# Optimization experiments

Hardware: AMD Instinct MI355X
Metric: run time of the kernel (lower is better)

The kernel has to match this reference:

```python
import jax, jax.numpy as jnp
import numpy as np

E = 1024      # embed_dim
QH = 16       # query heads
KVH = 4       # kv heads
HD = E // QH  # head_dim = 64
KVE = HD * KVH  # 256
EPS = 1e-5
ROPE_BASE = 10000.0


def rope(x, d):
    # Faithful to the source RoPE: d == number of heads (x.shape[-2]),
    # and the 'sequence' axis of the cache is x.shape[0] (the batch dim).
    # rope(x) = x*cos + (x*sin) * neg_half(x)  (note: nonlinear in x).
    b = x.shape[0]
    theta = 1.0 / (ROPE_BASE ** (jnp.arange(0, d, 2, dtype=jnp.float32) / d))  # (d//2,)
    seq_idx = jnp.arange(b, dtype=jnp.float32)                                 # (b,)
    idx_theta = seq_idx[:, None] * theta[None, :]                              # (b, d//2)
    idx2 = jnp.concatenate([idx_theta, idx_theta], axis=-1)                    # (b, d)
    # cached shape (b,1,1,d); source permutes (0,1,3,2) -> (b,1,d,1)
    cos = jnp.cos(idx2)[:, None, :, None]  # (b,1,d,1)
    sin = jnp.sin(idx2)[:, None, :, None]
    d2 = d // 2
    # split of the LAST dim (head_dim) at d//2 == num_heads//2, as in source
    neg = jnp.concatenate([-x[..., d2:], x[..., :d2]], axis=-1)
    return x * cos + (x * sin) * neg


def setup_inputs() -> dict:
    key = jax.random.key(0)
    ks = jax.random.split(key, 12)
    b, n = 1, 2048

    def xavier(k, shape):
        fan_out, fan_in = shape
        std = (2.0 / (fan_in + fan_out)) ** 0.5
        return jax.random.normal(k, shape, dtype=jnp.float32) * std

    return {
        "query": jax.random.normal(ks[0], (b, n, E), dtype=jnp.float32),
        "key": jax.random.normal(ks[1], (b, n, E), dtype=jnp.float32),
        "value": jax.random.normal(ks[2], (b, n, E), dtype=jnp.float32),
        "Wq": xavier(ks[3], (E, E)),
        "bq": jnp.zeros((E,), jnp.float32),
        "Wk": xavier(ks[4], (KVE, E)),
        "bk": jnp.zeros((KVE,), jnp.float32),
        "Wv": xavier(ks[5], (KVE, E)),
        "bv": jnp.zeros((KVE,), jnp.float32),
        "gamma": jnp.ones((E,), jnp.float32),
        "beta": jnp.zeros((E,), jnp.float32),
    }


def reference(query, key, value, Wq, bq, Wk, bk, Wv, bv, gamma, beta):
    b, n, _ = query.shape
    q = query @ Wq.T + bq            # (b,n,E)
    k = key @ Wk.T + bk              # (b,n,KVE)
    v = value @ Wv.T + bv            # (b,n,KVE)

    q = q.reshape(b, n, QH, HD)      # b n h d
    k = k.reshape(b, n, KVH, HD)
    v = v.reshape(b, n, KVH, HD)

    q = rope(q, QH)
    k = rope(k, KVH)

    # b n h d -> b h n d
    q = jnp.transpose(q, (0, 2, 1, 3))
    k = jnp.transpose(k, (0, 2, 1, 3))
    v = jnp.transpose(v, (0, 2, 1, 3))

    scale = float(HD) ** 0.5
    q = q / scale

    g = QH // KVH
    # 'b (h g) n d -> b g h n d' : h outer, g inner
    q = q.reshape(b, KVH, g, n, HD)              # (b, h, g, n, d)
    q = jnp.transpose(q, (0, 2, 1, 3, 4))        # (b, g, h, n, d)

    sim = jnp.einsum('bghnd,bhsd->bghns', q, k)  # (b,g,h,n,s)
    attn = jax.nn.softmax(sim, axis=-1)
    out = jnp.einsum('bghns,bhsd->bghnd', attn, v)

    # 'b g h n d -> b n (h g) d'
    out = jnp.transpose(out, (0, 3, 2, 1, 4))    # (b, n, h, g, d)
    x = out.reshape(b, n, QH * HD)               # (b, n, E)

    # LayerNorm (biased variance, as in torch)
    mu = jnp.mean(x, axis=-1, keepdims=True)
    var = jnp.mean((x - mu) ** 2, axis=-1, keepdims=True)
    x = (x - mu) * jax.lax.rsqrt(var + EPS) * gamma + beta

    # NOTE: source computes out_proj(x) but returns x, so out_proj is dead code.
    return x
```

## Files before the change

kernel.cpp:

```cpp
#include <hip/hip_runtime.h>
#include <math.h>

#define EDIM   1024
#define KVEDIM 256
#define HDIM   64
#define QHEADS 16

typedef __attribute__((ext_vector_type(8))) short short8;
typedef __attribute__((ext_vector_type(4))) float f32x4;

__device__ __forceinline__ unsigned pack2(float a, float b) {
    unsigned ua = __builtin_bit_cast(unsigned, a);
    unsigned ub = __builtin_bit_cast(unsigned, b);
    ua += 0x7fffu + ((ua >> 16) & 1u);
    ub += 0x7fffu + ((ub >> 16) & 1u);
    return (ua >> 16) | (ub & 0xffff0000u);
}
__device__ __forceinline__ short f2b(float a) {
    unsigned ua = __builtin_bit_cast(unsigned, a);
    ua += 0x7fffu + ((ua >> 16) & 1u);
    return (short)(ua >> 16);
}

__global__ __launch_bounds__(256)
void cvt_bf16(const float* __restrict__ s0, const float* __restrict__ s1,
              const float* __restrict__ s2, const float* __restrict__ s3,
              const float* __restrict__ s4, const float* __restrict__ s5,
              short* __restrict__ d0, short* __restrict__ d1,
              short* __restrict__ d2, short* __restrict__ d3,
              short* __restrict__ d4, short* __restrict__ d5,
              int n0, int n1, int n2, int n3, int n4, int n5)
{
    const float* s; short* d; int n;
    switch (blockIdx.y) {
        case 0: s = s0; d = d0; n = n0; break;
        case 1: s = s1; d = d1; n = n1; break;
        case 2: s = s2; d = d2; n = n2; break;
        case 3: s = s3; d = d3; n = n3; break;
        case 4: s = s4; d = d4; n = n4; break;
        default: s = s5; d = d5; n = n5; break;
    }
    int i = ((int)blockIdx.x * 256 + threadIdx.x) * 8;
    if (i >= n) return;
    float4 a = *(const float4*)&s[i];
    float4 b = *(const float4*)&s[i + 4];
    uint4 o;
    o.x = pack2(a.x, a.y); o.y = pack2(a.z, a.w);
    o.z = pack2(b.x, b.y); o.w = pack2(b.z, b.w);
    *(uint4*)&d[i] = o;
}

__global__ __launch_bounds__(256)
void proj_gemm(const short* __restrict__ Aq, const short* __restrict__ Ak,
               const short* __restrict__ Av,
               const short* __restrict__ Wqb, const short* __restrict__ Wkb,
               const short* __restrict__ Wvb,
               const float* __restrict__ bq, const float* __restrict__ bk,
               const float* __restrict__ bv,
               short* __restrict__ Cq, short* __restrict__ Ck,
               short* __restrict__ Cv, float qscale)
{
    const int bid = blockIdx.x;
    const short* A; const short* W; const float* bias; short* C;
    int N, bm, bn; float scale;
    if (bid < 128) {
        A = Aq; W = Wqb; bias = bq; C = Cq; N = EDIM; scale = qscale;
        bm = (bid >> 3) * 128; bn = (bid & 7) * 128;
    } else if (bid < 160) {
        int i = bid - 128;
        A = Ak; W = Wkb; bias = bk; C = Ck; N = KVEDIM; scale = 1.0f;
        bm = (i >> 1) * 128; bn = (i & 1) * 128;
    } else {
        int i = bid - 160;
        A = Av; W = Wvb; bias = bv; C = Cv; N = KVEDIM; scale = 1.0f;
        bm = (i >> 1) * 128; bn = (i & 1) * 128;
    }
    const int K = EDIM;

    __shared__ short As[128 * 72];
    __shared__ short Ws[128 * 72];

    const int t = threadIdx.x, lane = t & 63, wv = t >> 6;
    const int lm = lane & 15, quad = lane >> 4;
    const int q8 = quad * 8, q4 = quad * 4;
    const int wm = (wv & 1) * 64, wn = (wv >> 1) * 64;
    const int sr = t >> 3, sc = (t & 7) * 8;

    f32x4 zero = {0.f, 0.f, 0.f, 0.f};
    f32x4 acc[4][4];
    #pragma unroll
    for (int i = 0; i < 4; ++i)
        #pragma unroll
        for (int j = 0; j < 4; ++j) acc[i][j] = zero;

    for (int k0 = 0; k0 < K; k0 += 64) {
        __syncthreads();
        #pragma unroll
        for (int i = 0; i < 4; ++i) {
            int r = sr + i * 32;
            *(uint4*)&As[r * 72 + sc] = *(const uint4*)&A[(size_t)(bm + r) * K + k0 + sc];
            *(uint4*)&Ws[r * 72 + sc] = *(const uint4*)&W[(size_t)(bn + r) * K + k0 + sc];
        }
        __syncthreads();
        #pragma unroll
        for (int ks = 0; ks < 2; ++ks) {
            short8 af[4], bfr[4];
            #pragma unroll
            for (int i = 0; i < 4; ++i)
                af[i] = *(const short8*)&As[(wm + i * 16 + lm) * 72 + ks * 32 + q8];
            #pragma unroll
            for (int j = 0; j < 4; ++j)
                bfr[j] = *(const short8*)&Ws[(wn + j * 16 + lm) * 72 + ks * 32 + q8];
            #pragma unroll
            for (int i = 0; i < 4; ++i)
                #pragma unroll
                for (int j = 0; j < 4; ++j)
                    acc[i][j] = __builtin_amdgcn_mfma_f32_16x16x32_bf16(
                        af[i], bfr[j], acc[i][j], 0, 0, 0);
        }
    }

    #pragma unroll
    for (int j = 0; j < 4; ++j) {
        float bj = bias[bn + wn + j * 16 + lm];
        #pragma unroll
        for (int i = 0; i < 4; ++i)
            #pragma unroll
            for (int r = 0; r < 4; ++r)
                C[(size_t)(bm + wm + i * 16 + q4 + r) * N + bn + wn + j * 16 + lm] =
                    f2b((acc[i][j][r] + bj) * scale);
    }
}

__global__ __launch_bounds__(256)
void attn_mfma(const short* __restrict__ q, const short* __restrict__ k,
               const short* __restrict__ v, float* __restrict__ x, int n)
{
    __shared__ short Ks[64 * 72];
    __shared__ short Vt[64 * 72];
    __shared__ short Ps[64 * 72];
    __shared__ float Lred[4][64];

    const int qh = blockIdx.y, kvh = qh >> 2;
    const int r0 = blockIdx.x * 64;
    const int t = threadIdx.x;
    const int lane = t & 63, wv = t >> 6;
    const int lm = lane & 15, quad = lane >> 4;
    const int q8 = quad * 8, q4 = quad * 4;

    short8 qf[4][2];
    #pragma unroll
    for (int qt = 0; qt < 4; ++qt) {
        const short* qrow = &q[(size_t)(r0 + qt * 16 + lm) * EDIM + qh * HDIM];
        qf[qt][0] = *(const short8*)&qrow[q8];
        qf[qt][1] = *(const short8*)&qrow[32 + q8];
    }

    const int rt0 = (wv & 1) * 2;
    const int dt0 = (wv >> 1) * 2;

    f32x4 zero = {0.f, 0.f, 0.f, 0.f};
    f32x4 oacc[2][2];
    #pragma unroll
    for (int i = 0; i < 2; ++i)
        #pragma unroll
        for (int j = 0; j < 2; ++j) oacc[i][j] = zero;
    float lp[4] = {0.f, 0.f, 0.f, 0.f};

    const int krow = t >> 2, kc = (t & 3) * 8;
    const int vs4 = (t & 15) * 4, vd0 = (t >> 4) * 4;

    for (int s0 = 0; s0 < n; s0 += 64) {
        __syncthreads();
        {
            const uint4* ksrc = (const uint4*)&k[(size_t)(s0 + krow) * KVEDIM + kvh * HDIM];
            uint4 ka = ksrc[t & 3];
            uint4 kb = ksrc[(t & 3) + 4];
            *(uint4*)&Ks[krow * 72 + kc] = ka;
            *(uint4*)&Ks[krow * 72 + kc + 32] = kb;
        }
        {
            unsigned vr[4][2];
            #pragma unroll
            for (int i = 0; i < 4; ++i) {
                uint2 vv = *(const uint2*)&v[(size_t)(s0 + vs4 + i) * KVEDIM + kvh * HDIM + vd0];
                vr[i][0] = vv.x; vr[i][1] = vv.y;
            }
            #pragma unroll
            for (int j = 0; j < 4; ++j) {
                int w = j >> 1, hi = (j & 1) * 16;
                unsigned e0 = (vr[0][w] >> hi) & 0xffffu;
                unsigned e1 = (vr[1][w] >> hi) & 0xffffu;
                unsigned e2 = (vr[2][w] >> hi) & 0xffffu;
                unsigned e3 = (vr[3][w] >> hi) & 0xffffu;
                uint2 o; o.x = e0 | (e1 << 16); o.y = e2 | (e3 << 16);
                *(uint2*)&Vt[(vd0 + j) * 72 + vs4] = o;
            }
        }
        __syncthreads();

        short8 kf0 = *(const short8*)&Ks[(wv * 16 + lm) * 72 + q8];
        short8 kf1 = *(const short8*)&Ks[(wv * 16 + lm) * 72 + 32 + q8];
        #pragma unroll
        for (int qt = 0; qt < 4; ++qt) {
            f32x4 s = zero;
            s = __builtin_amdgcn_mfma_f32_16x16x32_bf16(kf0, qf[qt][0], s, 0, 0, 0);
            s = __builtin_amdgcn_mfma_f32_16x16x32_bf16(kf1, qf[qt][1], s, 0, 0, 0);
            float p0 = exp2f(s[0]);
            float p1 = exp2f(s[1]);
            float p2 = exp2f(s[2]);
            float p3 = exp2f(s[3]);
            lp[qt] += (p0 + p1) + (p2 + p3);
            uint2 pw; pw.x = pack2(p0, p1); pw.y = pack2(p2, p3);
            *(uint2*)&Ps[(qt * 16 + lm) * 72 + wv * 16 + q4] = pw;
        }
        __syncthreads();

        short8 vf[2][2];
        #pragma unroll
        for (int j = 0; j < 2; ++j) {
            vf[j][0] = *(const short8*)&Vt[((dt0 + j) * 16 + lm) * 72 + q8];
            vf[j][1] = *(const short8*)&Vt[((dt0 + j) * 16 + lm) * 72 + 32 + q8];
        }
        #pragma unroll
        for (int i = 0; i < 2; ++i) {
            short8 pf0 = *(const short8*)&Ps[((rt0 + i) * 16 + lm) * 72 + q8];
            short8 pf1 = *(const short8*)&Ps[((rt0 + i) * 16 + lm) * 72 + 32 + q8];
            #pragma unroll
            for (int j = 0; j < 2; ++j) {
                oacc[i][j] = __builtin_amdgcn_mfma_f32_16x16x32_bf16(pf0, vf[j][0], oacc[i][j], 0, 0, 0);
                oacc[i][j] = __builtin_amdgcn_mfma_f32_16x16x32_bf16(pf1, vf[j][1], oacc[i][j], 0, 0, 0);
            }
        }
    }

    #pragma unroll
    for (int qt = 0; qt < 4; ++qt) {
        float l = lp[qt];
        l += __shfl_xor(l, 16);
        l += __shfl_xor(l, 32);
        if (lane < 16) Lred[wv][qt * 16 + lm] = l;
    }
    __syncthreads();

    #pragma unroll
    for (int i = 0; i < 2; ++i) {
        #pragma unroll
        for (int r = 0; r < 4; ++r) {
            int row = (rt0 + i) * 16 + q4 + r;
            float lsum = (Lred[0][row] + Lred[1][row]) + (Lred[2][row] + Lred[3][row]);
            float inv = 1.0f / lsum;
            #pragma unroll
            for (int j = 0; j < 2; ++j)
                x[(size_t)(r0 + row) * EDIM + qh * HDIM + (dt0 + j) * 16 + lm] =
                    oacc[i][j][r] * inv;
        }
    }
}

__global__ __launch_bounds__(256)
void ln_kernel(float* __restrict__ x, const float* __restrict__ gamma,
               const float* __restrict__ beta)
{
    const int rowbase = (int)blockIdx.x * EDIM;
    const int t = threadIdx.x;

    float4 xv = *(const float4*)&x[rowbase + t * 4];
    float s  = xv.x + xv.y + xv.z + xv.w;
    float sq = xv.x * xv.x + xv.y * xv.y + xv.z * xv.z + xv.w * xv.w;
    #pragma unroll
    for (int m = 1; m < 64; m <<= 1) {
        s  += __shfl_xor(s,  m);
        sq += __shfl_xor(sq, m);
    }
    __shared__ float ws_[4], wq_[4];
    const int wave = t >> 6;
    if ((t & 63) == 0) { ws_[wave] = s; wq_[wave] = sq; }
    __syncthreads();
    s  = ws_[0] + ws_[1] + ws_[2] + ws_[3];
    sq = wq_[0] + wq_[1] + wq_[2] + wq_[3];

    const float mu   = s * (1.f / EDIM);
    const float var  = sq * (1.f / EDIM) - mu * mu;
    const float rstd = rsqrtf(var + 1e-5f);

    float4 g = *(const float4*)&gamma[t * 4];
    float4 b = *(const float4*)&beta[t * 4];
    float4 o;
    o.x = (xv.x - mu) * rstd * g.x + b.x;
    o.y = (xv.y - mu) * rstd * g.y + b.y;
    o.z = (xv.z - mu) * rstd * g.z + b.z;
    o.w = (xv.w - mu) * rstd * g.w + b.w;
    *(float4*)&x[rowbase + t * 4] = o;
}

extern "C" void kernel_launch(void* const* d_in, const int* in_sizes, int n_in,
                              void* d_out, int out_size, void* d_ws, size_t ws_size,
                              hipStream_t stream)
{
    const float* query = (const float*)d_in[0];
    const float* key   = (const float*)d_in[1];
    const float* value = (const float*)d_in[2];
    const float* Wq    = (const float*)d_in[3];
    const float* bq    = (const float*)d_in[4];
    const float* Wk    = (const float*)d_in[5];
    const float* bk    = (const float*)d_in[6];
    const float* Wv    = (const float*)d_in[7];
    const float* bv    = (const float*)d_in[8];
    const float* gamma = (const float*)d_in[9];
    const float* beta  = (const float*)d_in[10];
    float* out = (float*)d_out;

    const int n = in_sizes[0] / EDIM;

    short* qa  = (short*)d_ws;
    short* ka  = qa  + (size_t)n * EDIM;
    short* va  = ka  + (size_t)n * EDIM;
    short* wqb = va  + (size_t)n * EDIM;
    short* wkb = wqb + (size_t)EDIM * EDIM;
    short* wvb = wkb + (size_t)KVEDIM * EDIM;
    short* qb  = wvb + (size_t)KVEDIM * EDIM;
    short* kb  = qb  + (size_t)n * EDIM;
    short* vb  = kb  + (size_t)n * KVEDIM;

    const float qscale = 0.125f * 1.44269504088896f;

    cvt_bf16<<<dim3(1024, 6), 256, 0, stream>>>(
        query, key, value, Wq, Wk, Wv,
        qa, ka, va, wqb, wkb, wvb,
        n * EDIM, n * EDIM, n * EDIM, EDIM * EDIM, KVEDIM * EDIM, KVEDIM * EDIM);

    proj_gemm<<<dim3(192), 256, 0, stream>>>(
        qa, ka, va, wqb, wkb, wvb, bq, bk, bv, qb, kb, vb, qscale);

    attn_mfma<<<dim3(n / 64, QHEADS), 256, 0, stream>>>(qb, kb, vb, out, n);

    ln_kernel<<<dim3(n), 256, 0, stream>>>(out, gamma, beta);
}
```

Measured before the change: 176.1 us.

## Split attention over key segments, prefetch K/V and GEMM tiles into registers

The attention kernel now splits the key sequence into two segments across a third grid dimension, which doubles the block count (512 to 1024). Each segment writes unnormalized partial outputs and row sums, and the LayerNorm kernel is replaced by one that combines the segments before normalizing. The attention and projection GEMM loops both prefetch the next tile's global loads into registers while the current tile is computed, and exp2f is swapped for the hardware exp2 builtin. The cost is extra partial-output traffic (two fp32 n×E buffers) and more workspace. The max-free softmax is unchanged, so summing segments stays exact.

```diff
diff --git a/kernel.cpp b/kernel.cpp
--- a/kernel.cpp
+++ b/kernel.cpp
@@ -5,6 +5,7 @@
 #define KVEDIM 256
 #define HDIM   64
 #define QHEADS 16
+#define NSEG   2
 
 typedef __attribute__((ext_vector_type(8))) short short8;
 typedef __attribute__((ext_vector_type(4))) float f32x4;
@@ -21,6 +22,12 @@
     ua += 0x7fffu + ((ua >> 16) & 1u);
     return (short)(ua >> 16);
 }
+
+#if __has_builtin(__builtin_amdgcn_exp2f)
+__device__ __forceinline__ float fexp2(float x) { return __builtin_amdgcn_exp2f(x); }
+#else
+__device__ __forceinline__ float fexp2(float x) { return exp2f(x); }
+#endif
 
 __global__ __launch_bounds__(256)
 void cvt_bf16(const float* __restrict__ s0, const float* __restrict__ s1,
@@ -84,7 +91,11 @@
     const int lm = lane & 15, quad = lane >> 4;
     const int q8 = quad * 8, q4 = quad * 4;
     const int wm = (wv & 1) * 64, wn = (wv >> 1) * 64;
-    const int sr = t >> 3, sc = (t & 7) * 8;
+
+    const int ar = t >> 1;
+    const int ac = (t & 1) * 32;
+    const short* Abase = A + (size_t)(bm + ar) * K + ac;
+    const short* Wbase = W + (size_t)(bn + ar) * K + ac;
 
     f32x4 zero = {0.f, 0.f, 0.f, 0.f};
     f32x4 acc[4][4];
@@ -93,30 +104,43 @@
         #pragma unroll
         for (int j = 0; j < 4; ++j) acc[i][j] = zero;
 
+    uint4 pa[4], pw[4];
+    #pragma unroll
+    for (int u = 0; u < 4; ++u) {
+        pa[u] = *(const uint4*)(Abase + u * 8);
+        pw[u] = *(const uint4*)(Wbase + u * 8);
+    }
+
     for (int k0 = 0; k0 < K; k0 += 64) {
         __syncthreads();
         #pragma unroll
-        for (int i = 0; i < 4; ++i) {
-            int r = sr + i * 32;
-            *(uint4*)&As[r * 72 + sc] = *(const uint4*)&A[(size_t)(bm + r) * K + k0 + sc];
-            *(uint4*)&Ws[r * 72 + sc] = *(const uint4*)&W[(size_t)(bn + r) * K + k0 + sc];
+        for (int u = 0; u < 4; ++u) {
+            *(uint4*)&As[ar * 72 + ac + u * 8] = pa[u];
+            *(uint4*)&Ws[ar * 72 + ac + u * 8] = pw[u];
         }
         __syncthreads();
+        if (k0 + 64 < K) {
+            #pragma unroll
+            for (int u = 0; u < 4; ++u) {
+                pa[u] = *(const uint4*)(Abase + k0 + 64 + u * 8);
+                pw[u] = *(const uint4*)(Wbase + k0 + 64 + u * 8);
+            }
+        }
         #pragma unroll
         for (int ks = 0; ks < 2; ++ks) {
-            short8 af[4], bfr[4];
+            short8 af[4], wf[4];
             #pragma unroll
             for (int i = 0; i < 4; ++i)
                 af[i] = *(const short8*)&As[(wm + i * 16 + lm) * 72 + ks * 32 + q8];
             #pragma unroll
             for (int j = 0; j < 4; ++j)
-                bfr[j] = *(const short8*)&Ws[(wn + j * 16 + lm) * 72 + ks * 32 + q8];
+                wf[j] = *(const short8*)&Ws[(wn + j * 16 + lm) * 72 + ks * 32 + q8];
             #pragma unroll
             for (int i = 0; i < 4; ++i)
                 #pragma unroll
                 for (int j = 0; j < 4; ++j)
                     acc[i][j] = __builtin_amdgcn_mfma_f32_16x16x32_bf16(
-                        af[i], bfr[j], acc[i][j], 0, 0, 0);
+                        af[i], wf[j], acc[i][j], 0, 0, 0);
         }
     }
 
@@ -134,7 +158,8 @@
 
 __global__ __launch_bounds__(256)
 void attn_mfma(const short* __restrict__ q, const short* __restrict__ k,
-               const short* __restrict__ v, float* __restrict__ x, int n)
+               const short* __restrict__ v, float* __restrict__ Opart,
+               float* __restrict__ Lpart, int n)
 {
     __shared__ short Ks[64 * 72];
     __shared__ short Vt[64 * 72];
@@ -143,6 +168,9 @@
 
     const int qh = blockIdx.y, kvh = qh >> 2;
     const int r0 = blockIdx.x * 64;
+    const int seg = blockIdx.z;
+    const int segkeys = n / NSEG;
+    const int sbeg = seg * segkeys;
     const int t = threadIdx.x;
     const int lane = t & 63, wv = t >> 6;
     const int lm = lane & 15, quad = lane >> 4;
@@ -170,34 +198,51 @@
     const int krow = t >> 2, kc = (t & 3) * 8;
     const int vs4 = (t & 15) * 4, vd0 = (t >> 4) * 4;
 
-    for (int s0 = 0; s0 < n; s0 += 64) {
+    uint4 kp0, kp1; uint2 vp[4];
+    {
+        const uint4* ksrc = (const uint4*)&k[(size_t)(sbeg + krow) * KVEDIM + kvh * HDIM];
+        kp0 = ksrc[t & 3];
+        kp1 = ksrc[(t & 3) + 4];
+        #pragma unroll
+        for (int i = 0; i < 4; ++i)
+            vp[i] = *(const uint2*)&v[(size_t)(sbeg + vs4 + i) * KVEDIM + kvh * HDIM + vd0];
+    }
+
+    for (int c = 0; c < segkeys; c += 64) {
         __syncthreads();
+        *(uint4*)&Ks[krow * 72 + kc] = kp0;
+        *(uint4*)&Ks[krow * 72 + kc + 32] = kp1;
         {
-            const uint4* ksrc = (const uint4*)&k[(size_t)(s0 + krow) * KVEDIM + kvh * HDIM];
-            uint4 ka = ksrc[t & 3];
-            uint4 kb = ksrc[(t & 3) + 4];
-            *(uint4*)&Ks[krow * 72 + kc] = ka;
-            *(uint4*)&Ks[krow * 72 + kc + 32] = kb;
-        }
-        {
-            unsigned vr[4][2];
-            #pragma unroll
-            for (int i = 0; i < 4; ++i) {
-                uint2 vv = *(const uint2*)&v[(size_t)(s0 + vs4 + i) * KVEDIM + kvh * HDIM + vd0];
-                vr[i][0] = vv.x; vr[i][1] = vv.y;
-            }
+            unsigned vr0 = vp[0].x, vr0b = vp[0].y;
+            unsigned vr1 = vp[1].x, vr1b = vp[1].y;
+            unsigned vr2 = vp[2].x, vr2b = vp[2].y;
+            unsigned vr3 = vp[3].x, vr3b = vp[3].y;
             #pragma unroll
             for (int j = 0; j < 4; ++j) {
-                int w = j >> 1, hi = (j & 1) * 16;
-                unsigned e0 = (vr[0][w] >> hi) & 0xffffu;
-                unsigned e1 = (vr[1][w] >> hi) & 0xffffu;
-                unsigned e2 = (vr[2][w] >> hi) & 0xffffu;
-                unsigned e3 = (vr[3][w] >> hi) & 0xffffu;
+                unsigned a = (j >> 1) ? vr0b : vr0;
+                unsigned b = (j >> 1) ? vr1b : vr1;
+                unsigned cc = (j >> 1) ? vr2b : vr2;
+                unsigned d = (j >> 1) ? vr3b : vr3;
+                int hi = (j & 1) * 16;
+                unsigned e0 = (a >> hi) & 0xffffu;
+                unsigned e1 = (b >> hi) & 0xffffu;
+                unsigned e2 = (cc >> hi) & 0xffffu;
+                unsigned e3 = (d >> hi) & 0xffffu;
                 uint2 o; o.x = e0 | (e1 << 16); o.y = e2 | (e3 << 16);
                 *(uint2*)&Vt[(vd0 + j) * 72 + vs4] = o;
             }
         }
         __syncthreads();
+
+        if (c + 64 < segkeys) {
+            const int s1 = sbeg + c + 64;
+            const uint4* ksrc = (const uint4*)&k[(size_t)(s1 + krow) * KVEDIM + kvh * HDIM];
+            kp0 = ksrc[t & 3];
+            kp1 = ksrc[(t & 3) + 4];
+            #pragma unroll
+            for (int i = 0; i < 4; ++i)
+                vp[i] = *(const uint2*)&v[(size_t)(s1 + vs4 + i) * KVEDIM + kvh * HDIM + vd0];
+        }
 
         short8 kf0 = *(const short8*)&Ks[(wv * 16 + lm) * 72 + q8];
         short8 kf1 = *(const short8*)&Ks[(wv * 16 + lm) * 72 + 32 + q8];
@@ -206,10 +251,10 @@
             f32x4 s = zero;
             s = __builtin_amdgcn_mfma_f32_16x16x32_bf16(kf0, qf[qt][0], s, 0, 0, 0);
             s = __builtin_amdgcn_mfma_f32_16x16x32_bf16(kf1, qf[qt][1], s, 0, 0, 0);
-            float p0 = exp2f(s[0]);
-            float p1 = exp2f(s[1]);
-            float p2 = exp2f(s[2]);
-            float p3 = exp2f(s[3]);
+            float p0 = fexp2(s[0]);
+            float p1 = fexp2(s[1]);
+            float p2 = fexp2(s[2]);
+            float p3 = fexp2(s[3]);
             lp[qt] += (p0 + p1) + (p2 + p3);
             uint2 pw; pw.x = pack2(p0, p1); pw.y = pack2(p2, p3);
             *(uint2*)&Ps[(qt * 16 + lm) * 72 + wv * 16 + q4] = pw;
@@ -249,25 +294,46 @@
         for (int r = 0; r < 4; ++r) {
             int row = (rt0 + i) * 16 + q4 + r;
             float lsum = (Lred[0][row] + Lred[1][row]) + (Lred[2][row] + Lred[3][row]);
-            float inv = 1.0f / lsum;
+            if (dt0 == 0 && lm == 0)
+                Lpart[((size_t)seg * n + r0 + row) * QHEADS + qh] = lsum;
             #pragma unroll
             for (int j = 0; j < 2; ++j)
-                x[(size_t)(r0 + row) * EDIM + qh * HDIM + (dt0 + j) * 16 + lm] =
-                    oacc[i][j][r] * inv;
+                Opart[((size_t)seg * n + r0 + row) * EDIM + qh * HDIM + (dt0 + j) * 16 + lm] =
+                    oacc[i][j][r];
         }
     }
 }
 
 __global__ __launch_bounds__(256)
-void ln_kernel(float* __restrict__ x, const float* __restrict__ gamma,
-               const float* __restrict__ beta)
+void combine_ln(const float* __restrict__ Opart, const float* __restrict__ Lpart,
+                const float* __restrict__ gamma, const float* __restrict__ beta,
+                float* __restrict__ out, int n)
 {
-    const int rowbase = (int)blockIdx.x * EDIM;
+    const int r = blockIdx.x;
     const int t = threadIdx.x;
 
-    float4 xv = *(const float4*)&x[rowbase + t * 4];
-    float s  = xv.x + xv.y + xv.z + xv.w;
-    float sq = xv.x * xv.x + xv.y * xv.y + xv.z * xv.z + xv.w * xv.w;
+    __shared__ float linv[QHEADS];
+    if (t < QHEADS) {
+        float l = 0.f;
+        #pragma unroll
+        for (int s = 0; s < NSEG; ++s)
+            l += Lpart[((size_t)s * n + r) * QHEADS + t];
+        linv[t] = 1.0f / l;
+    }
+    __syncthreads();
+
+    const int c = t * 4;
+    float4 o = {0.f, 0.f, 0.f, 0.f};
+    #pragma unroll
+    for (int s = 0; s < NSEG; ++s) {
+        float4 p = *(const float4*)&Opart[((size_t)s * n + r) * EDIM + c];
+        o.x += p.x; o.y += p.y; o.z += p.z; o.w += p.w;
+    }
+    const float inv = linv[c >> 6];
+    o.x *= inv; o.y *= inv; o.z *= inv; o.w *= inv;
+
+    float s  = o.x + o.y + o.z + o.w;
+    float sq = o.x * o.x + o.y * o.y + o.z * o.z + o.w * o.w;
     #pragma unroll
     for (int m = 1; m < 64; m <<= 1) {
         s  += __shfl_xor(s,  m);
@@ -284,14 +350,14 @@
     const float var  = sq * (1.f / EDIM) - mu * mu;
     const float rstd = rsqrtf(var + 1e-5f);
 
-    float4 g = *(const float4*)&gamma[t * 4];
-    float4 b = *(const float4*)&beta[t * 4];
-    float4 o;
-    o.x = (xv.x - mu) * rstd * g.x + b.x;
-    o.y = (xv.y - mu) * rstd * g.y + b.y;
-    o.z = (xv.z - mu) * rstd * g.z + b.z;
-    o.w = (xv.w - mu) * rstd * g.w + b.w;
-    *(float4*)&x[rowbase + t * 4] = o;
+    float4 g = *(const float4*)&gamma[c];
+    float4 b = *(const float4*)&beta[c];
+    float4 y;
+    y.x = (o.x - mu) * rstd * g.x + b.x;
+    y.y = (o.y - mu) * rstd * g.y + b.y;
+    y.z = (o.z - mu) * rstd * g.z + b.z;
+    y.w = (o.w - mu) * rstd * g.w + b.w;
+    *(float4*)&out[(size_t)r * EDIM + c] = y;
 }
 
 extern "C" void kernel_launch(void* const* d_in, const int* in_sizes, int n_in,
@@ -322,6 +388,8 @@
     short* qb  = wvb + (size_t)KVEDIM * EDIM;
     short* kb  = qb  + (size_t)n * EDIM;
     short* vb  = kb  + (size_t)n * KVEDIM;
+    float* Opart = (float*)(vb + (size_t)n * KVEDIM);
+    float* Lpart = Opart + (size_t)NSEG * n * EDIM;
 
     const float qscale = 0.125f * 1.44269504088896f;
 
@@ -333,7 +401,8 @@
     proj_gemm<<<dim3(192), 256, 0, stream>>>(
         qa, ka, va, wqb, wkb, wvb, bq, bk, bv, qb, kb, vb, qscale);
 
-    attn_mfma<<<dim3(n / 64, QHEADS), 256, 0, stream>>>(qb, kb, vb, out, n);
-
-    ln_kernel<<<dim3(n), 256, 0, stream>>>(out, gamma, beta);
-}
+    attn_mfma<<<dim3(n / 64, QHEADS, NSEG), 256, 0, stream>>>(
+        qb, kb, vb, Opart, Lpart, n);
+
+    combine_ln<<<dim3(n), 256, 0, stream>>>(Opart, Lpart, gamma, beta, out, n);
+}
```

Result: slower. 204.8 us (+16.3%).
